# Kernel tuning notes

Hardware: AMD Instinct MI355X
Metric: run time of the kernel (lower is better)

The kernel has to match this reference:

```python
import jax, jax.numpy as jnp
import numpy as np

N, C, T, V = 32, 128, 128, 25
HS, HT, CI = 3, 2, 32
BN_INV = float(1.0 / np.sqrt(1.0 + 1e-5))  # eval-mode BN: running_mean=0, running_var=1


def conv1x1(x, w, b):
    # x: (N,C,T,V), w: (O,C), b: (O,)
    return jnp.einsum('nctv,oc->notv', x, w) + b[None, :, None, None]


def bn(x, g, b):
    return x * (g * BN_INV)[None, :, None, None] + b[None, :, None, None]


def lrelu(x):
    return jax.nn.leaky_relu(x, 0.1)


def setup_inputs() -> dict:
    key = jax.random.key(0)
    ks = jax.random.split(key, 16)
    w = lambda k, shp: jax.random.normal(k, shp, dtype=jnp.float32) * 0.05
    inp = {
        'x': jax.random.normal(ks[0], (N, C, T, V), dtype=jnp.float32),
        # spatial attention QK projection (conv 1x1): 2*HS*CI out channels
        'w_in_s': w(ks[1], (2 * HS * CI, C)), 'b_in_s': jnp.zeros((2 * HS * CI,), jnp.float32),
        'attention0s': jnp.ones((1, HS, V, V), jnp.float32) / V,
        'alphas': jnp.ones((1, HS, 1, 1), jnp.float32),
        'w_out_s': w(ks[2], (C, HS * C)), 'b_out_s': jnp.zeros((C,), jnp.float32),
        'g_out_s': jnp.ones((C,), jnp.float32), 'be_out_s': jnp.zeros((C,), jnp.float32),
        'w_ff_s': w(ks[3], (C, C)), 'b_ff_s': jnp.zeros((C,), jnp.float32),
        'g_ff_s': jnp.ones((C,), jnp.float32), 'be_ff_s': jnp.zeros((C,), jnp.float32),
        # temporal attention QK projection: 4*HT*CI out channels
        'w_in_t': w(ks[4], (4 * HT * CI, C)), 'b_in_t': jnp.zeros((4 * HT * CI,), jnp.float32),
        'alphat_f': jnp.ones((1, HT, 1, 1), jnp.float32),
        'alphat_b': jnp.ones((1, HT, 1, 1), jnp.float32),
        'w_out_t': w(ks[5], (C, 2 * HT * C)), 'b_out_t': jnp.zeros((C,), jnp.float32),
        'g_out_t': jnp.ones((C,), jnp.float32), 'be_out_t': jnp.zeros((C,), jnp.float32),
        'w_ff_t': w(ks[6], (C, C)), 'b_ff_t': jnp.zeros((C,), jnp.float32),
        'g_ff_t': jnp.ones((C,), jnp.float32), 'be_ff_t': jnp.zeros((C,), jnp.float32),
        # TCN: 7x1 temporal conv
        'w_tcn': w(ks[7], (C, C, 7, 1)), 'b_tcn': jnp.zeros((C,), jnp.float32),
        'g_tcn': jnp.ones((C,), jnp.float32), 'be_tcn': jnp.zeros((C,), jnp.float32),
    }
    return inp


def reference(x, w_in_s, b_in_s, attention0s, alphas, w_out_s, b_out_s, g_out_s, be_out_s,
              w_ff_s, b_ff_s, g_ff_s, be_ff_s, w_in_t, b_in_t, alphat_f, alphat_b,
              w_out_t, b_out_t, g_out_t, be_out_t, w_ff_t, b_ff_t, g_ff_t, be_ff_t,
              w_tcn, b_tcn, g_tcn, be_tcn):
    n = x.shape[0]
    # ---------------- spatial attention (S_atten='free', glo_reg_s) ----------------
    att_bias = attention0s[:, :, None]            # (1,HS,1,V,V) broadcast over T
    alphas_u = alphas[:, :, None]                 # (1,HS,1,1,1)
    qk = conv1x1(x, w_in_s, b_in_s).reshape(n, 2 * HS, CI, T, V)
    q, k = qk[:, :HS], qk[:, HS:]
    att = att_bias + jnp.tanh(jnp.einsum('nsctu,nsctv->nstuv', q, k) / CI) * alphas_u  # (N,HS,T,V,V)
    y = jnp.einsum('nctu,nstuv->nsctv', x, att).reshape(n, HS * C, T, V)
    y = bn(conv1x1(y, w_out_s, b_out_s), g_out_s, be_out_s)
    y = lrelu(x + y)                               # downs1 = identity (in==out, stride 1)
    y = bn(conv1x1(y, w_ff_s, b_ff_s), g_ff_s, be_ff_s)
    s_out = lrelu(x + y)                           # downs2 = identity
    # ---------------- temporal attention (directed, T_atten='context') ----------------
    z_in = s_out                                   # parallel=False -> temporal eats s_out
    qk_t = conv1x1(z_in, w_in_t, b_in_t).reshape(n, 4 * HT, CI, T, V)
    qt, kt = qk_t[:, :2 * HT], qk_t[:, 2 * HT:]
    qt = qt.mean(-1)                               # context attention: mean over joints -> (N,2HT,CI,T)
    kt = kt.mean(-1)
    att_t = jnp.tanh(jnp.einsum('nsct,nscu->nstu', qt, kt) / CI)  # (N,2HT,T,T)
    backward_mask = jnp.triu(jnp.ones((T, T), jnp.float32))
    forward_mask = backward_mask.T
    att_f = att_t[:, :HT] * alphat_f * forward_mask
    att_b = att_t[:, HT:] * alphat_b * backward_mask
    att_t = jnp.concatenate([att_f, att_b], axis=1)               # (N,2HT,T,T)
    z = jnp.einsum('nctv,nstu->nscuv', z_in, att_t).reshape(n, 2 * HT * C, T, V)
    z = bn(conv1x1(z, w_out_t, b_out_t), g_out_t, be_out_t)
    z = lrelu(z_in + z)                            # downt1 = identity
    z = bn(conv1x1(z, w_ff_t, b_ff_t), g_ff_t, be_ff_t)
    t_out = lrelu(z_in + z)                        # downt2 = identity
    # ---------------- TCN branch ----------------
    z2 = jax.lax.conv_general_dilated(t_out, w_tcn, (1, 1), ((3, 3), (0, 0)),
                                      dimension_numbers=('NCHW', 'OIHW', 'NCHW'))
    z2 = bn(z2 + b_tcn[None, :, None, None] * 0 + b_tcn[None, :, None, None], g_tcn, be_tcn) if False else bn(z2 + b_tcn[None, :, None, None], g_tcn, be_tcn)
    out = lrelu(t_out + z2)                        # downtTCN = identity
    return out
```

## Files before the change

### kernel.cpp

```cpp
#include <hip/hip_runtime.h>
#include <cstddef>

#define Nn 32
#define Cc 128
#define Tt 128
#define Vv 25
#define BN_INV 0.9999950000374997f


typedef __attribute__((ext_vector_type(8))) short bf16x8;
typedef __attribute__((ext_vector_type(4))) float f32x4;

__device__ __forceinline__ unsigned short f2bf(float f) {
    union { float f; unsigned u; } x; x.f = f;
    return (unsigned short)((x.u + 0x7FFFu + ((x.u >> 16) & 1u)) >> 16);
}
__device__ __forceinline__ float bf2f(unsigned short s) {
    union { unsigned u; float f; } x; x.u = ((unsigned)s) << 16;
    return x.f;
}


#define GFETCH(K0)                                                             \
    {                                                                          \
        int mg = m0 + sm;                                                      \
        if (mg < M) {                                                          \
            const unsigned short* ap = An + (size_t)mg*lda + (K0) + skh*16;    \
            a0n = *(const bf16x8*)ap;                                          \
            a1n = *(const bf16x8*)(ap + 8);                                    \
        }                                                                      \
        if (BMODE == 0) {                                                      \
            const unsigned short* Bn = (const unsigned short*)Bv               \
                                     + (size_t)n*bn_stride;                    \
            _Pragma("unroll")                                                  \
            for (int j = 0; j < 8; ++j)                                        \
                bqn[j] = Bn[(size_t)((K0) + skq*8 + j)*ldb + bcol];            \
        } else if (BMODE == 4) {                                               \
            const float* Bf = (const float*)Bv + (size_t)n*bn_stride;          \
            _Pragma("unroll")                                                  \
            for (int j = 0; j < 8; ++j)                                        \
                bqn[j] = f2bf(Bf[(size_t)((K0) + skq*8 + j)*ldb + bcol]);      \
        } else if (BMODE == 1) {                                               \
            const unsigned short* Bn = (const unsigned short*)Bv               \
                                     + (size_t)n*bn_stride;                    \
            int kb = (K0) + skq*8;                                             \
            int kidx = kb >> 7, c0 = kb & 127;                                 \
            int e = bcol + (kidx - 3)*25;                                      \
            bool ok = ((unsigned)e < 3200u);                                   \
            _Pragma("unroll")                                                  \
            for (int j = 0; j < 8; ++j)                                        \
                bqn[j] = ok ? Bn[(size_t)(c0 + j)*3200 + e] : (unsigned short)0;\
        } else {                                                  \
            const unsigned short* Bn = (const unsigned short*)Bv               \
                                     + (size_t)n*bn_stride;                    \
            int kb = (K0) + skq*8;                                             \
            int h = kb >> 7, t0b = kb & 127;                                   \
            const unsigned short* bp = Bn + (size_t)h*409600 + (size_t)bo*3200 \
                                          + (size_t)t0b*25 + bv_;              \
            _Pragma("unroll")                                                  \
            for (int j = 0; j < 8; ++j) bqn[j] = bp[j*25];                     \
        }                                                                      \
    }

template<int BMODE, int DMODE, int OM>
__global__ __launch_bounds__(256, 4) void gemm_k(
    const unsigned short* __restrict__ A, const void* __restrict__ Bv,
    float* __restrict__ D, unsigned short* __restrict__ Dbf,
    const float* __restrict__ resp, const float* __restrict__ bias,
    const float* __restrict__ gg, const float* __restrict__ bb,
    int M, int K, int lda, int ldb, int ldd,
    long an_stride, long bn_stride, long dn_stride, int gn)
{
    __shared__ short Al[8*64*8];
    __shared__ short Bl[4*64*8];

    const int n  = blockIdx.y;
    const int mt = blockIdx.x / gn;
    const int nt = blockIdx.x - mt*gn;
    const int m0 = mt*128;
    const int j0 = nt*64;

    const unsigned short* An = A + (size_t)n*an_stride;

    const int tid = threadIdx.x;
    const int wav = tid >> 6, lane = tid & 63;
    const int lq = lane >> 4, l16 = lane & 15;

    const int sm  = tid >> 1, skh = tid & 1;
    const int scol = tid & 63, skq = tid >> 6;
    const int bcol = j0 + scol;

    int bo = 0, bv_ = 0;
    if (BMODE == 3) { bo = bcol/25; bv_ = bcol - 25*bo; }

    f32x4 acc[2][4];
    #pragma unroll
    for (int i = 0; i < 2; ++i)
        #pragma unroll
        for (int c = 0; c < 4; ++c) acc[i][c] = (f32x4){0.f,0.f,0.f,0.f};

    bf16x8 a0n = (bf16x8){0,0,0,0,0,0,0,0}, a1n = a0n;
    unsigned short bqn[8];
    GFETCH(0);

    for (int k0 = 0; k0 < K; k0 += 32) {
        __syncthreads();
        {
            short* Ap = Al + ((size_t)((sm>>4)*64 + (sm&15) + 32*skh))*8;
            *(bf16x8*)Ap = a0n;
            *(bf16x8*)(Ap + 128) = a1n;
        }
        {
            short* Bp = Bl + ((size_t)((scol>>4)*64 + skq*16 + (scol&15)))*8;
            bf16x8 p0;
            #pragma unroll
            for (int j = 0; j < 8; ++j) p0[j] = (short)bqn[j];
            *(bf16x8*)Bp = p0;
        }
        __syncthreads();

        if (k0 + 32 < K) GFETCH(k0 + 32);

        bf16x8 afr[2], bfr[4];
        afr[0] = *(const bf16x8*)(Al + ((size_t)((2*wav+0)*64 + lane))*8);
        afr[1] = *(const bf16x8*)(Al + ((size_t)((2*wav+1)*64 + lane))*8);
        #pragma unroll
        for (int c = 0; c < 4; ++c)
            bfr[c] = *(const bf16x8*)(Bl + ((size_t)(c*64 + lane))*8);
        #pragma unroll
        for (int i = 0; i < 2; ++i)
            #pragma unroll
            for (int c = 0; c < 4; ++c)
                acc[i][c] = __builtin_amdgcn_mfma_f32_16x16x32_bf16(
                    afr[i], bfr[c], acc[i][c], 0, 0, 0);
    }

    #pragma unroll
    for (int i = 0; i < 2; ++i) {
        const int mbase = m0 + (2*wav + i)*16 + lq*4;
        #pragma unroll
        for (int ct = 0; ct < 4; ++ct) {
            const int col = j0 + ct*16 + l16;
            if (DMODE == 0) {
                #pragma unroll
                for (int r = 0; r < 4; ++r) {
                    const int mg = mbase + r;
                    if (mg < M) {
                        const size_t addr = (size_t)mg*ldd + col + (size_t)n*dn_stride;
                        float val = acc[i][ct][r] + (bias ? bias[mg] : 0.f);
                        if (gg) {
                            val = val*(gg[mg]*BN_INV) + bb[mg] + resp[addr];
                            val = val > 0.f ? val : 0.1f*val;
                        }
                        if (OM != 1) D[addr] = val;
                        if (OM >= 1) Dbf[addr] = f2bf(val);
                    }
                }
            } else {
                const int c = col/25, v = col - 25*c;
                const float bi = bias ? bias[c] : 0.f;
                float gv = 0.f, b2 = 0.f;
                if (gg) { gv = gg[c]*BN_INV; b2 = bb[c]; }
                #pragma unroll
                for (int r = 0; r < 4; ++r) {
                    const int u = mbase + r;
                    const size_t addr = (size_t)c*3200 + (size_t)u*25 + v
                                      + (size_t)n*dn_stride;
                    float val = acc[i][ct][r] + bi;
                    if (gg) {
                        val = val*gv + b2 + resp[addr];
                        val = val > 0.f ? val : 0.1f*val;
                    }
                    if (OM != 1) D[addr] = val;
                    if (OM >= 1) Dbf[addr] = f2bf(val);
                }
            }
        }
    }
}

__global__ void k_prep(const float* __restrict__ wis, const float* __restrict__ wos,
                       const float* __restrict__ wfs, const float* __restrict__ wit,
                       const float* __restrict__ wot, const float* __restrict__ wft,
                       const float* __restrict__ wtc, unsigned short* __restrict__ W) {
    int i = blockIdx.x*256 + threadIdx.x;
    if (i < 24576) { W[i] = f2bf(wis[i]); return; }          i -= 24576;
    if (i < 49152) { W[24576 + i] = f2bf(wos[i]); return; }  i -= 49152;
    if (i < 16384) { W[73728 + i] = f2bf(wfs[i]); return; }  i -= 16384;
    if (i < 32768) { W[90112 + i] = f2bf(wit[i]); return; }  i -= 32768;
    if (i < 65536) {
        int ho = i >> 7, c = i & 127; int h = ho >> 7, o = ho & 127;
        W[122880 + i] = f2bf(wot[o*512 + h*128 + c]); return; } i -= 65536;
    if (i < 16384) { W[188416 + i] = f2bf(wft[i]); return; } i -= 16384;
    if (i < 114688) {
        int o = i / 896; int r = i - o*896; int kidx = r >> 7, c = r & 127;
        W[204800 + i] = f2bf(wtc[(o*128 + c)*7 + kidx]); }
}

__global__ void k_att_s(const unsigned short* __restrict__ qk,
                        const float* __restrict__ att0,
                        const float* __restrict__ alphas,
                        unsigned short* __restrict__ att) {
    int b = blockIdx.x;
    int n = b / (3*Tt); int rem = b - n*(3*Tt); int s = rem / Tt; int t = rem - s*Tt;
    __shared__ float qs[32*Vv], ks[32*Vv];
    const unsigned short* qp = qk + (size_t)n*614400 + (size_t)(s*32)*3200 + t*25;
    const unsigned short* kp = qk + (size_t)n*614400 + (size_t)(96 + s*32)*3200 + t*25;
    for (int i = threadIdx.x; i < 32*Vv; i += 256) {
        int c = i / Vv, v = i - c*Vv;
        qs[i] = bf2f(qp[(size_t)c*3200 + v]);
        ks[i] = bf2f(kp[(size_t)c*3200 + v]);
    }
    __syncthreads();
    float alpha = alphas[s];
    for (int i = threadIdx.x; i < Vv*Vv; i += 256) {
        int u = i / Vv, v = i - u*Vv;
        float a = 0.f;
        #pragma unroll
        for (int c = 0; c < 32; ++c) a += qs[c*Vv + u] * ks[c*Vv + v];
        att[(size_t)n*240000 + (size_t)s*80000 + (size_t)t*625 + i] =
            f2bf(att0[s*625 + i] + tanhf(a * (1.f/32.f)) * alpha);
    }
}

__global__ __launch_bounds__(256, 2) void k_eins_mfma(
    const float* __restrict__ X, const unsigned short* __restrict__ att,
    unsigned short* __restrict__ y2)
{
    __shared__ short Xf[128*128];
    __shared__ short Bf[7*4*64*8];

    const int n  = blockIdx.x >> 5;
    const int t0 = (blockIdx.x & 31) * 4;
    const int tid = threadIdx.x;
    const int wav = tid >> 6, lane = tid & 63;
    const int lq = lane >> 4, l16 = lane & 15;

    for (int i = tid; i < 7*4*64; i += 256)
        *(bf16x8*)(Bf + (size_t)i*8) = (bf16x8){0,0,0,0,0,0,0,0};

    const float* xp = X + (size_t)n*409600;
    for (int i = tid; i < 8192; i += 256) {
        int u2 = (i & 15)*2, tl = (i >> 4) & 3, c = i >> 6;
        float f0 = 0.f, f1 = 0.f;
        if (u2 < 25) {
            const float* p = xp + (size_t)c*3200 + (t0 + tl)*25 + u2;
            f0 = p[0];
            if (u2 < 24) f1 = p[1];
        }
        unsigned pk = (unsigned)f2bf(f0) | ((unsigned)f2bf(f1) << 16);
        int byte = (i*4) ^ ((c & 7) << 4);
        *(unsigned*)((char*)Xf + byte) = pk;
    }
    __syncthreads();

    bf16x8 afr[2][4];
    #pragma unroll
    for (int i = 0; i < 2; ++i) {
        const int c = (2*wav + i)*16 + l16;
        #pragma unroll
        for (int ks = 0; ks < 4; ++ks) {
            int byte = ((c*128 + ks*32 + lq*8)*2) ^ ((c & 7) << 4);
            afr[i][ks] = *(const bf16x8*)((const char*)Xf + byte);
        }
    }

    for (int s = 0; s < 3; ++s) {
        const unsigned short* ap = att + (size_t)n*240000 + (size_t)s*80000
                                       + (size_t)t0*625;
        for (int j = tid; j < 2500; j += 256) {
            int tl = j / 625, r = j - tl*625;
            int u = r / 25, v = r - u*25;
            int col = tl*25 + v;
            int l = ((u >> 3) << 4) | (col & 15);
            int nt = col >> 4;
            Bf[(size_t)((nt*4 + tl)*64 + l)*8 + (u & 7)] = (short)ap[j];
        }
        __syncthreads();

        f32x4 acc[2][7];
        #pragma unroll
        for (int i = 0; i < 2; ++i)
            #pragma unroll
            for (int nt = 0; nt < 7; ++nt) acc[i][nt] = (f32x4){0.f,0.f,0.f,0.f};

        #pragma unroll
        for (int ks = 0; ks < 4; ++ks) {
            bf16x8 bfr[7];
            #pragma unroll
            for (int nt = 0; nt < 7; ++nt)
                bfr[nt] = *(const bf16x8*)(Bf + (size_t)((nt*4 + ks)*64 + lane)*8);
            #pragma unroll
            for (int i = 0; i < 2; ++i)
                #pragma unroll
                for (int nt = 0; nt < 7; ++nt)
                    acc[i][nt] = __builtin_amdgcn_mfma_f32_16x16x32_bf16(
                        afr[i][ks], bfr[nt], acc[i][nt], 0, 0, 0);
        }

        unsigned short* yb = y2 + (size_t)n*1228800 + (size_t)(s*128)*3200 + t0*25;
        #pragma unroll
        for (int i = 0; i < 2; ++i) {
            const int row = (2*wav + i)*16 + lq*4;
            #pragma unroll
            for (int nt = 0; nt < 7; ++nt) {
                const int col = nt*16 + l16;
                if (col < 100) {
                    unsigned short* yp = yb + (size_t)row*3200 + col;
                    #pragma unroll
                    for (int r = 0; r < 4; ++r)
                        yp[(size_t)r*3200] = f2bf(acc[i][nt][r]);
                }
            }
        }
        __syncthreads();
    }
}

__global__ void k_mean(const float* __restrict__ X, unsigned short* __restrict__ xb) {
    int idx = blockIdx.x*256 + threadIdx.x;
    if (idx >= Nn*Cc*Tt) return;
    const float* p = X + (size_t)idx*25;
    float s = 0.f;
    #pragma unroll
    for (int v = 0; v < Vv; ++v) s += p[v];
    xb[idx] = f2bf(s * (1.f/25.f));
}

__global__ void k_att_t(const float* __restrict__ qkt, const float* __restrict__ af,
                        const float* __restrict__ ab, unsigned short* __restrict__ attb) {
    int n = blockIdx.x >> 2, h = blockIdx.x & 3;
    __shared__ float qs[32*Tt], ks[32*Tt];
    const float* qp = qkt + (size_t)n*32768 + (size_t)(h*32)*128;
    const float* kp = qkt + (size_t)n*32768 + (size_t)(128 + h*32)*128;
    for (int i = threadIdx.x; i < 32*Tt; i += 256) { qs[i] = qp[i]; ks[i] = kp[i]; }
    __syncthreads();
    float alpha = (h < 2) ? af[h] : ab[h-2];
    for (int i = threadIdx.x; i < Tt*Tt; i += 256) {
        int u = i >> 7, t = i & 127;
        bool keep = (h < 2) ? (t >= u) : (t <= u);
        float val = 0.f;
        if (keep) {
            float a = 0.f;
            #pragma unroll
            for (int c = 0; c < 32; ++c) a += qs[c*Tt + t] * ks[c*Tt + u];
            val = tanhf(a * (1.f/32.f)) * alpha;
        }
        attb[(size_t)n*65536 + (size_t)u*512 + h*128 + t] = f2bf(val);
    }
}

extern "C" void kernel_launch(void* const* d_in, const int* in_sizes, int n_in,
                              void* d_out, int out_size, void* d_ws, size_t ws_size,
                              hipStream_t stream) {
    const float* x       = (const float*)d_in[0];
    const float* w_in_s  = (const float*)d_in[1];
    const float* b_in_s  = (const float*)d_in[2];
    const float* att0s   = (const float*)d_in[3];
    const float* alphas  = (const float*)d_in[4];
    const float* w_out_s = (const float*)d_in[5];
    const float* b_out_s = (const float*)d_in[6];
    const float* g_out_s = (const float*)d_in[7];
    const float* be_out_s= (const float*)d_in[8];
    const float* w_ff_s  = (const float*)d_in[9];
    const float* b_ff_s  = (const float*)d_in[10];
    const float* g_ff_s  = (const float*)d_in[11];
    const float* be_ff_s = (const float*)d_in[12];
    const float* w_in_t  = (const float*)d_in[13];
    const float* b_in_t  = (const float*)d_in[14];
    const float* alphat_f= (const float*)d_in[15];
    const float* alphat_b= (const float*)d_in[16];
    const float* w_out_t = (const float*)d_in[17];
    const float* b_out_t = (const float*)d_in[18];
    const float* g_out_t = (const float*)d_in[19];
    const float* be_out_t= (const float*)d_in[20];
    const float* w_ff_t  = (const float*)d_in[21];
    const float* b_ff_t  = (const float*)d_in[22];
    const float* g_ff_t  = (const float*)d_in[23];
    const float* be_ff_t = (const float*)d_in[24];
    const float* w_tcn   = (const float*)d_in[25];
    const float* b_tcn   = (const float*)d_in[26];
    const float* g_tcn   = (const float*)d_in[27];
    const float* be_tcn  = (const float*)d_in[28];

    hipMemsetAsync(d_ws, 0, ws_size, stream);

    float* ws = (float*)d_ws;
    unsigned short* WB    = (unsigned short*)ws;
    unsigned short* QKBF  = (unsigned short*)(ws + 200000);
    unsigned short* S1BF  = (unsigned short*)(ws + 200000);
    unsigned short* ATSB  = (unsigned short*)(ws + 10030400);
    unsigned short* Y2BF  = (unsigned short*)(ws + 13870400);
    float*          SOUT  = ws + 33531200;
    unsigned short* ATTB  = (unsigned short*)(ws + 200000);
    unsigned short* XBARB = (unsigned short*)(ws + 1300000);
    float*          QKT   = ws + 1600000;
    unsigned short* TMPB  = (unsigned short*)(ws + 2700000);
    unsigned short* T1BF  = (unsigned short*)(ws + 46638400);
    float*          TOUT  = ws + 2700000;
    unsigned short* TOUTB = (unsigned short*)(ws + 15810000);
    float* out = (float*)d_out;

    unsigned short* wbis = WB;
    unsigned short* wbos = WB + 24576;
    unsigned short* wbfs = WB + 73728;
    unsigned short* wbit = WB + 90112;
    unsigned short* wbot = WB + 122880;
    unsigned short* wbft = WB + 188416;
    unsigned short* wbtc = WB + 204800;

    dim3 blk(256);
    const float* NUL = nullptr;

    k_prep<<<1248, blk, 0, stream>>>(w_in_s, w_out_s, w_ff_s, w_in_t,
                                     w_out_t, w_ff_t, w_tcn, WB);

    gemm_k<4,0,1><<<dim3(100,32), blk, 0, stream>>>(
        wbis, x, nullptr, QKBF, NUL, b_in_s, NUL, NUL,
        192, 128, 128, 3200, 3200, 0L, 409600L, 614400L, 50);
    k_att_s<<<Nn*3*Tt, blk, 0, stream>>>(QKBF, att0s, alphas, ATSB);
    k_eins_mfma<<<dim3(Nn*32), blk, 0, stream>>>(x, ATSB, Y2BF);
    gemm_k<0,0,1><<<dim3(50,32), blk, 0, stream>>>(
        wbos, Y2BF, nullptr, S1BF, x, b_out_s, g_out_s, be_out_s,
        128, 384, 384, 3200, 3200, 0L, 1228800L, 409600L, 50);
    gemm_k<0,0,0><<<dim3(50,32), blk, 0, stream>>>(
        wbfs, S1BF, SOUT, nullptr, x, b_ff_s, g_ff_s, be_ff_s,
        128, 128, 128, 3200, 3200, 0L, 409600L, 409600L, 50);

    k_mean<<<2048, blk, 0, stream>>>(SOUT, XBARB);
    gemm_k<0,0,0><<<dim3(4,32), blk, 0, stream>>>(
        wbit, XBARB, QKT, nullptr, NUL, b_in_t, NUL, NUL,
        256, 128, 128, 128, 128, 0L, 16384L, 32768L, 2);
    k_att_t<<<Nn*4, blk, 0, stream>>>(QKT, alphat_f, alphat_b, ATTB);
    gemm_k<4,0,1><<<dim3(200,32), blk, 0, stream>>>(
        wbot, SOUT, nullptr, TMPB, NUL, NUL, NUL, NUL,
        512, 128, 128, 3200, 3200, 0L, 409600L, 1638400L, 50);
    gemm_k<3,2,1><<<dim3(50,32), blk, 0, stream>>>(
        ATTB, TMPB, nullptr, T1BF, SOUT, b_out_t, g_out_t, be_out_t,
        128, 512, 512, 3200, 3200, 65536L, 1638400L, 409600L, 50);
    gemm_k<0,0,2><<<dim3(50,32), blk, 0, stream>>>(
        wbft, T1BF, TOUT, TOUTB, SOUT, b_ff_t, g_ff_t, be_ff_t,
        128, 128, 128, 3200, 3200, 0L, 409600L, 409600L, 50);

    gemm_k<1,0,0><<<dim3(50,32), blk, 0, stream>>>(
        wbtc, TOUTB, out, nullptr, TOUT, b_tcn, g_tcn, be_tcn,
        128, 896, 896, 3200, 3200, 0L, 409600L, 409600L, 50);
}
```

Measured before the change: 767.7 us.

## Widen GEMM tiles to 128 columns, double-buffer LDS, drop workspace memset

The generic MFMA GEMM kernel now computes 128x128 output tiles instead of 128x64, with each thread fetching 16 B-rows per step. It uses two LDS buffers, so global prefetch, staging and compute overlap with one barrier per half-step instead of two per step. Launch bounds drop to 2 blocks per SM to allow the larger accumulator, and all grid sizes are halved to match. The full-workspace hipMemsetAsync is removed as well, which assumes no kernel relies on zero-initialised scratch. The cost is lower occupancy from higher register and LDS use.

```diff
diff --git a/kernel.cpp b/kernel.cpp
--- a/kernel.cpp
+++ b/kernel.cpp
@@ -21,49 +21,79 @@
 }
 
 
-#define GFETCH(K0)                                                             \
+#define GFETCH(K0, A0r, A1r, BQr)                                              \
     {                                                                          \
         int mg = m0 + sm;                                                      \
         if (mg < M) {                                                          \
             const unsigned short* ap = An + (size_t)mg*lda + (K0) + skh*16;    \
-            a0n = *(const bf16x8*)ap;                                          \
-            a1n = *(const bf16x8*)(ap + 8);                                    \
+            A0r = *(const bf16x8*)ap;                                          \
+            A1r = *(const bf16x8*)(ap + 8);                                    \
         }                                                                      \
         if (BMODE == 0) {                                                      \
             const unsigned short* Bn = (const unsigned short*)Bv               \
                                      + (size_t)n*bn_stride;                    \
             _Pragma("unroll")                                                  \
-            for (int j = 0; j < 8; ++j)                                        \
-                bqn[j] = Bn[(size_t)((K0) + skq*8 + j)*ldb + bcol];            \
+            for (int j = 0; j < 16; ++j)                                       \
+                BQr[j] = Bn[(size_t)((K0) + skq*16 + j)*ldb + bcol];           \
         } else if (BMODE == 4) {                                               \
             const float* Bf = (const float*)Bv + (size_t)n*bn_stride;          \
             _Pragma("unroll")                                                  \
-            for (int j = 0; j < 8; ++j)                                        \
-                bqn[j] = f2bf(Bf[(size_t)((K0) + skq*8 + j)*ldb + bcol]);      \
+            for (int j = 0; j < 16; ++j)                                       \
+                BQr[j] = f2bf(Bf[(size_t)((K0) + skq*16 + j)*ldb + bcol]);     \
         } else if (BMODE == 1) {                                               \
             const unsigned short* Bn = (const unsigned short*)Bv               \
                                      + (size_t)n*bn_stride;                    \
-            int kb = (K0) + skq*8;                                             \
+            int kb = (K0) + skq*16;                                            \
             int kidx = kb >> 7, c0 = kb & 127;                                 \
             int e = bcol + (kidx - 3)*25;                                      \
             bool ok = ((unsigned)e < 3200u);                                   \
             _Pragma("unroll")                                                  \
-            for (int j = 0; j < 8; ++j)                                        \
-                bqn[j] = ok ? Bn[(size_t)(c0 + j)*3200 + e] : (unsigned short)0;\
+            for (int j = 0; j < 16; ++j)                                       \
+                BQr[j] = ok ? Bn[(size_t)(c0 + j)*3200 + e] : (unsigned short)0;\
         } else {                                                  \
             const unsigned short* Bn = (const unsigned short*)Bv               \
                                      + (size_t)n*bn_stride;                    \
-            int kb = (K0) + skq*8;                                             \
+            int kb = (K0) + skq*16;                                            \
             int h = kb >> 7, t0b = kb & 127;                                   \
             const unsigned short* bp = Bn + (size_t)h*409600 + (size_t)bo*3200 \
                                           + (size_t)t0b*25 + bv_;              \
             _Pragma("unroll")                                                  \
-            for (int j = 0; j < 8; ++j) bqn[j] = bp[j*25];                     \
+            for (int j = 0; j < 16; ++j) BQr[j] = bp[j*25];                    \
         }                                                                      \
     }
 
+#define STAGE(BUF, A0r, A1r, BQr)                                              \
+    {                                                                          \
+        short* Ap = Al[BUF] + ((size_t)((sm>>4)*64 + (sm&15) + 32*skh))*8;     \
+        *(bf16x8*)Ap = A0r;                                                    \
+        *(bf16x8*)(Ap + 128) = A1r;                                            \
+        short* Bp = Bl[BUF] + ((size_t)((scol>>4)*64 + (scol&15) + 32*skq))*8; \
+        bf16x8 p0, p1;                                                         \
+        _Pragma("unroll")                                                      \
+        for (int j = 0; j < 8; ++j) { p0[j] = (short)BQr[j];                   \
+                                      p1[j] = (short)BQr[8+j]; }               \
+        *(bf16x8*)Bp = p0;                                                     \
+        *(bf16x8*)(Bp + 128) = p1;                                             \
+    }
+
+#define COMP(BUF)                                                              \
+    {                                                                          \
+        bf16x8 afr[2], bfr[8];                                                 \
+        afr[0] = *(const bf16x8*)(Al[BUF] + ((size_t)((2*wav+0)*64 + lane))*8);\
+        afr[1] = *(const bf16x8*)(Al[BUF] + ((size_t)((2*wav+1)*64 + lane))*8);\
+        _Pragma("unroll")                                                      \
+        for (int c = 0; c < 8; ++c)                                            \
+            bfr[c] = *(const bf16x8*)(Bl[BUF] + ((size_t)(c*64 + lane))*8);    \
+        _Pragma("unroll")                                                      \
+        for (int i = 0; i < 2; ++i)                                            \
+            _Pragma("unroll")                                                  \
+            for (int c = 0; c < 8; ++c)                                        \
+                acc[i][c] = __builtin_amdgcn_mfma_f32_16x16x32_bf16(           \
+                    afr[i], bfr[c], acc[i][c], 0, 0, 0);                       \
+    }
+
 template<int BMODE, int DMODE, int OM>
-__global__ __launch_bounds__(256, 4) void gemm_k(
+__global__ __launch_bounds__(256, 2) void gemm_k(
     const unsigned short* __restrict__ A, const void* __restrict__ Bv,
     float* __restrict__ D, unsigned short* __restrict__ Dbf,
     const float* __restrict__ resp, const float* __restrict__ bias,
@@ -71,14 +101,14 @@
     int M, int K, int lda, int ldb, int ldd,
     long an_stride, long bn_stride, long dn_stride, int gn)
 {
-    __shared__ short Al[8*64*8];
-    __shared__ short Bl[4*64*8];
+    __shared__ short Al[2][8*64*8];
+    __shared__ short Bl[2][8*64*8];
 
     const int n  = blockIdx.y;
     const int mt = blockIdx.x / gn;
     const int nt = blockIdx.x - mt*gn;
     const int m0 = mt*128;
-    const int j0 = nt*64;
+    const int j0 = nt*128;
 
     const unsigned short* An = A + (size_t)n*an_stride;
 
@@ -87,59 +117,44 @@
     const int lq = lane >> 4, l16 = lane & 15;
 
     const int sm  = tid >> 1, skh = tid & 1;
-    const int scol = tid & 63, skq = tid >> 6;
+    const int scol = tid & 127, skq = tid >> 7;
     const int bcol = j0 + scol;
 
     int bo = 0, bv_ = 0;
     if (BMODE == 3) { bo = bcol/25; bv_ = bcol - 25*bo; }
 
-    f32x4 acc[2][4];
+    f32x4 acc[2][8];
     #pragma unroll
     for (int i = 0; i < 2; ++i)
         #pragma unroll
-        for (int c = 0; c < 4; ++c) acc[i][c] = (f32x4){0.f,0.f,0.f,0.f};
-
-    bf16x8 a0n = (bf16x8){0,0,0,0,0,0,0,0}, a1n = a0n;
-    unsigned short bqn[8];
-    GFETCH(0);
-
-    for (int k0 = 0; k0 < K; k0 += 32) {
+        for (int c = 0; c < 8; ++c) acc[i][c] = (f32x4){0.f,0.f,0.f,0.f};
+
+    bf16x8 a0A = (bf16x8){0,0,0,0,0,0,0,0}, a1A = a0A;
+    bf16x8 a0B = a0A, a1B = a0A;
+    unsigned short bqA[16], bqB[16];
+
+    GFETCH(0,  a0A, a1A, bqA);
+    GFETCH(32, a0B, a1B, bqB);
+    STAGE(0, a0A, a1A, bqA);
+    __syncthreads();
+
+    for (int k0 = 0; k0 < K; k0 += 64) {
+        if (k0 + 64 < K) GFETCH(k0 + 64, a0A, a1A, bqA);
+        STAGE(1, a0B, a1B, bqB);
+        COMP(0);
         __syncthreads();
-        {
-            short* Ap = Al + ((size_t)((sm>>4)*64 + (sm&15) + 32*skh))*8;
-            *(bf16x8*)Ap = a0n;
-            *(bf16x8*)(Ap + 128) = a1n;
-        }
-        {
-            short* Bp = Bl + ((size_t)((scol>>4)*64 + skq*16 + (scol&15)))*8;
-            bf16x8 p0;
-            #pragma unroll
-            for (int j = 0; j < 8; ++j) p0[j] = (short)bqn[j];
-            *(bf16x8*)Bp = p0;
-        }
+
+        if (k0 + 96 < K) GFETCH(k0 + 96, a0B, a1B, bqB);
+        if (k0 + 64 < K) STAGE(0, a0A, a1A, bqA);
+        COMP(1);
         __syncthreads();
-
-        if (k0 + 32 < K) GFETCH(k0 + 32);
-
-        bf16x8 afr[2], bfr[4];
-        afr[0] = *(const bf16x8*)(Al + ((size_t)((2*wav+0)*64 + lane))*8);
-        afr[1] = *(const bf16x8*)(Al + ((size_t)((2*wav+1)*64 + lane))*8);
-        #pragma unroll
-        for (int c = 0; c < 4; ++c)
-            bfr[c] = *(const bf16x8*)(Bl + ((size_t)(c*64 + lane))*8);
-        #pragma unroll
-        for (int i = 0; i < 2; ++i)
-            #pragma unroll
-            for (int c = 0; c < 4; ++c)
-                acc[i][c] = __builtin_amdgcn_mfma_f32_16x16x32_bf16(
-                    afr[i], bfr[c], acc[i][c], 0, 0, 0);
     }
 
     #pragma unroll
     for (int i = 0; i < 2; ++i) {
         const int mbase = m0 + (2*wav + i)*16 + lq*4;
         #pragma unroll
-        for (int ct = 0; ct < 4; ++ct) {
+        for (int ct = 0; ct < 8; ++ct) {
             const int col = j0 + ct*16 + l16;
             if (DMODE == 0) {
                 #pragma unroll
@@ -383,8 +398,6 @@
     const float* g_tcn   = (const float*)d_in[27];
     const float* be_tcn  = (const float*)d_in[28];
 
-    hipMemsetAsync(d_ws, 0, ws_size, stream);
-
     float* ws = (float*)d_ws;
     unsigned short* WB    = (unsigned short*)ws;
     unsigned short* QKBF  = (unsigned short*)(ws + 200000);
@@ -415,34 +428,34 @@
     k_prep<<<1248, blk, 0, stream>>>(w_in_s, w_out_s, w_ff_s, w_in_t,
                                      w_out_t, w_ff_t, w_tcn, WB);
 
-    gemm_k<4,0,1><<<dim3(100,32), blk, 0, stream>>>(
+    gemm_k<4,0,1><<<dim3(50,32), blk, 0, stream>>>(
         wbis, x, nullptr, QKBF, NUL, b_in_s, NUL, NUL,
-        192, 128, 128, 3200, 3200, 0L, 409600L, 614400L, 50);
+        192, 128, 128, 3200, 3200, 0L, 409600L, 614400L, 25);
     k_att_s<<<Nn*3*Tt, blk, 0, stream>>>(QKBF, att0s, alphas, ATSB);
     k_eins_mfma<<<dim3(Nn*32), blk, 0, stream>>>(x, ATSB, Y2BF);
-    gemm_k<0,0,1><<<dim3(50,32), blk, 0, stream>>>(
+    gemm_k<0,0,1><<<dim3(25,32), blk, 0, stream>>>(
         wbos, Y2BF, nullptr, S1BF, x, b_out_s, g_out_s, be_out_s,
-        128, 384, 384, 3200, 3200, 0L, 1228800L, 409600L, 50);
-    gemm_k<0,0,0><<<dim3(50,32), blk, 0, stream>>>(
+        128, 384, 384, 3200, 3200, 0L, 1228800L, 409600L, 25);
+    gemm_k<0,0,0><<<dim3(25,32), blk, 0, stream>>>(
         wbfs, S1BF, SOUT, nullptr, x, b_ff_s, g_ff_s, be_ff_s,
-        128, 128, 128, 3200, 3200, 0L, 409600L, 409600L, 50);
+        128, 128, 128, 3200, 3200, 0L, 409600L, 409600L, 25);
 
     k_mean<<<2048, blk, 0, stream>>>(SOUT, XBARB);
-    gemm_k<0,0,0><<<dim3(4,32), blk, 0, stream>>>(
+    gemm_k<0,0,0><<<dim3(2,32), blk, 0, stream>>>(
         wbit, XBARB, QKT, nullptr, NUL, b_in_t, NUL, NUL,
-        256, 128, 128, 128, 128, 0L, 16384L, 32768L, 2);
+        256, 128, 128, 128, 128, 0L, 16384L, 32768L, 1);
     k_att_t<<<Nn*4, blk, 0, stream>>>(QKT, alphat_f, alphat_b, ATTB);
-    gemm_k<4,0,1><<<dim3(200,32), blk, 0, stream>>>(
+    gemm_k<4,0,1><<<dim3(100,32), blk, 0, stream>>>(
         wbot, SOUT, nullptr, TMPB, NUL, NUL, NUL, NUL,
-        512, 128, 128, 3200, 3200, 0L, 409600L, 1638400L, 50);
-    gemm_k<3,2,1><<<dim3(50,32), blk, 0, stream>>>(
+        512, 128, 128, 3200, 3200, 0L, 409600L, 1638400L, 25);
+    gemm_k<3,2,1><<<dim3(25,32), blk, 0, stream>>>(
         ATTB, TMPB, nullptr, T1BF, SOUT, b_out_t, g_out_t, be_out_t,
-        128, 512, 512, 3200, 3200, 65536L, 1638400L, 409600L, 50);
-    gemm_k<0,0,2><<<dim3(50,32), blk, 0, stream>>>(
+        128, 512, 512, 3200, 3200, 65536L, 1638400L, 409600L, 25);
+    gemm_k<0,0,2><<<dim3(25,32), blk, 0, stream>>>(
         wbft, T1BF, TOUT, TOUTB, SOUT, b_ff_t, g_ff_t, be_ff_t,
-        128, 128, 128, 3200, 3200, 0L, 409600L, 409600L, 50);
-
-    gemm_k<1,0,0><<<dim3(50,32), blk, 0, stream>>>(
+        128, 128, 128, 3200, 3200, 0L, 409600L, 409600L, 25);
+
+    gemm_k<1,0,0><<<dim3(25,32), blk, 0, stream>>>(
         wbtc, TOUTB, out, nullptr, TOUT, b_tcn, g_tcn, be_tcn,
-        128, 896, 896, 3200, 3200, 0L, 409600L, 409600L, 50);
-}
+        128, 896, 896, 3200, 3200, 0L, 409600L, 409600L, 25);
+}
```

After: 940.3 us. +22.5%, slower.
